# Performance work log

Hardware: AMD Instinct MI355X
Metric: run time of the kernel (lower is better)

The kernel has to match this reference:

```python
import jax, jax.numpy as jnp
import numpy as np

B, T, IN, H, NC = 2048, 128, 64, 256, 1


def setup_inputs() -> dict:
    key = jax.random.key(0)
    ks = jax.random.split(key, 7)
    s_ih = 1.0 / np.sqrt(H)
    return {
        "x": jax.random.normal(ks[0], (B, T, IN), dtype=jnp.float32),
        "W_ih": jax.random.normal(ks[1], (4 * H, IN), dtype=jnp.float32) * s_ih,
        "W_hh": jax.random.normal(ks[2], (4 * H, H), dtype=jnp.float32) * s_ih,
        "b_ih": jax.random.normal(ks[3], (4 * H,), dtype=jnp.float32) * s_ih,
        "b_hh": jax.random.normal(ks[4], (4 * H,), dtype=jnp.float32) * s_ih,
        "fc_W": jax.random.normal(ks[5], (NC, H), dtype=jnp.float32) * s_ih,
        "fc_b": jax.random.normal(ks[6], (NC,), dtype=jnp.float32) * s_ih,
    }


def _lstm_last_hidden(x, W_ih, W_hh, b_ih, b_hh):
    # Precompute input contribution for all timesteps: [B, T, 4H]
    xg = jnp.einsum('bti,gi->btg', x, W_ih) + (b_ih + b_hh)
    h0 = jnp.zeros((x.shape[0], H), dtype=x.dtype)
    c0 = jnp.zeros((x.shape[0], H), dtype=x.dtype)

    def step(carry, xg_t):
        h, c = carry
        gates = xg_t + h @ W_hh.T  # [B, 4H], PyTorch gate order i,f,g,o
        i, f, g, o = jnp.split(gates, 4, axis=-1)
        i = jax.nn.sigmoid(i)
        f = jax.nn.sigmoid(f)
        g = jnp.tanh(g)
        o = jax.nn.sigmoid(o)
        c = f * c + i * g
        h = o * jnp.tanh(c)
        return (h, c), None

    (h_last, _), _ = jax.lax.scan(step, (h0, c0), jnp.swapaxes(xg, 0, 1))
    return h_last  # [B, H]


def reference(x, W_ih, W_hh, b_ih, b_hh, fc_W, fc_b):
    h_last = _lstm_last_hidden(x, W_ih, W_hh, b_ih, b_hh)
    return h_last @ fc_W.T + fc_b  # [B, num_classes]
```

## Files before the change

kernel.cpp:

```cpp
#include <hip/hip_runtime.h>

typedef _Float16 half8 __attribute__((ext_vector_type(8)));
typedef float f32x4 __attribute__((ext_vector_type(4)));
typedef unsigned int u32x2 __attribute__((ext_vector_type(2)));

#define B_SZ   2048
#define T_SZ   128
#define IN_SZ  64
#define H_SZ   256
#define G4     1024
#define NB     8
#define NGRP   32
#define NTHR   512
#define KT_N   10
#define HPAD   36

__device__ __forceinline__ float sigmoidf_(float x) { return 1.0f / (1.0f + __expf(-x)); }
__device__ __forceinline__ float tanhf_(float x) { return 1.0f - 2.0f / (__expf(2.0f * x) + 1.0f); }

__global__ void prep_kernel(const float* __restrict__ W_ih, const float* __restrict__ W_hh,
                            const float* __restrict__ b_ih, const float* __restrict__ b_hh,
                            _Float16* __restrict__ Wr, float* __restrict__ biasr) {
  const int tid = blockIdx.x * blockDim.x + threadIdx.x;
  if (tid < G4) {
    const int TI = tid >> 4, m = tid & 15;
    const int q = m & 3, cs = m >> 2, nbk = TI >> 3, sub = TI & 7;
    const int grow = q * 256 + nbk * 32 + sub * 4 + cs;
    biasr[tid] = b_ih[grow] + b_hh[grow];
  }
  if (tid >= 64 * KT_N * 64) return;
  const int l = tid & 63, kt = (tid >> 6) % KT_N, TI = tid / (64 * KT_N);
  const int lm = l & 15, lk = l >> 4;
  const int q = lm & 3, cs = lm >> 2, nbk = TI >> 3, sub = TI & 7;
  const int grow = q * 256 + nbk * 32 + sub * 4 + cs;
  const int k0 = kt * 32 + lk * 8;
  _Float16 v[8];
  #pragma unroll
  for (int kk = 0; kk < 8; ++kk) {
    const int k = k0 + kk;
    v[kk] = (_Float16)((k < IN_SZ) ? W_ih[grow * IN_SZ + k] : W_hh[grow * H_SZ + k - IN_SZ]);
  }
  *(half8*)&Wr[((size_t)(TI * KT_N + kt) * 64 + l) * 8] = *(half8*)v;
}

__global__ __launch_bounds__(NTHR, 1)
void lstm_kernel(const float* __restrict__ x,
                 const _Float16* __restrict__ Wr,
                 const float* __restrict__ biasr,
                 const float* __restrict__ fcW,
                 _Float16* __restrict__ hbuf,
                 int* __restrict__ flags,
                 float* __restrict__ partial) {
  __shared__ __align__(16) _Float16 Wlds[8 * KT_N * 512];
  __shared__ __align__(16) _Float16 hslab[64][HPAD];

  const int tid = threadIdx.x;
  const int l = tid & 63;
  const int w = tid >> 6;
  const int lm = l & 15, lk = l >> 4;
  const int bt = w & 3, gh = w >> 2;
  const int g = blockIdx.x >> 3, nbk = blockIdx.x & 7;
  const int brow = g * 64 + bt * 16 + lm;

  #pragma unroll
  for (int rep = 0; rep < 10; ++rep) {
    const int u = rep * NTHR + tid;
    const int sub = u / 640, r2 = u % 640, kt = r2 >> 6, l2 = r2 & 63;
    *(half8*)&Wlds[((size_t)(sub * KT_N + kt) * 64 + l2) * 8] =
        *(const half8*)&Wr[(((size_t)(nbk * 8 + sub) * KT_N + kt) * 64 + l2) * 8];
  }

  f32x4 bias[4];
  #pragma unroll
  for (int ti = 0; ti < 4; ++ti)
    bias[ti] = *(const f32x4*)&biasr[(nbk * 8 + gh * 4 + ti) * 16 + lk * 4];

  const float* xlane = x + (size_t)brow * T_SZ * IN_SZ + lk * 8;
  const int hcolb = gh * 16 + lk;
  int* flagg = flags + g * T_SZ;

  __syncthreads();

  float cst[4] = {0.f, 0.f, 0.f, 0.f};

  #define WL(ti_, kt_) (*(const half8*)&Wlds[((size_t)((gh * 4 + (ti_)) * KT_N + (kt_)) * 64 + l) * 8])

  for (int t = 0; t < T_SZ; ++t) {
    const int par = t & 1;

    half8 bx0, bx1;
    {
      const float* xp = xlane + t * IN_SZ;
      const f32x4 a0 = *(const f32x4*)(xp);
      const f32x4 a1 = *(const f32x4*)(xp + 4);
      const f32x4 b0 = *(const f32x4*)(xp + 32);
      const f32x4 b1 = *(const f32x4*)(xp + 36);
      #pragma unroll
      for (int i = 0; i < 4; ++i) {
        bx0[i] = (_Float16)a0[i]; bx0[4 + i] = (_Float16)a1[i];
        bx1[i] = (_Float16)b0[i]; bx1[4 + i] = (_Float16)b1[i];
      }
    }

    f32x4 acc[4];
    #pragma unroll
    for (int ti = 0; ti < 4; ++ti) acc[ti] = bias[ti];

    #pragma unroll
    for (int ti = 0; ti < 4; ++ti)
      acc[ti] = __builtin_amdgcn_mfma_f32_16x16x32_f16(WL(ti, 0), bx0, acc[ti], 0, 0, 0);
    #pragma unroll
    for (int ti = 0; ti < 4; ++ti)
      acc[ti] = __builtin_amdgcn_mfma_f32_16x16x32_f16(WL(ti, 1), bx1, acc[ti], 0, 0, 0);

    if (t > 0) {
      if (tid == 0) {
        while (__hip_atomic_load(flagg + (t - 1), __ATOMIC_RELAXED, __HIP_MEMORY_SCOPE_AGENT) < NB)
          __builtin_amdgcn_s_sleep(2);
      }
      __syncthreads();

      const char* hb = (const char*)hbuf + (size_t)(par ^ 1) * (B_SZ * H_SZ * 2)
                       + (size_t)brow * (H_SZ * 2) + lk * 16;
      f32x4 hr0, hr1, hr2, hr3, hr4, hr5, hr6, hr7;
      asm volatile("global_load_dwordx4 %0, %1, off sc0 sc1"            : "=v"(hr0) : "v"(hb));
      asm volatile("global_load_dwordx4 %0, %1, off offset:64 sc0 sc1"  : "=v"(hr1) : "v"(hb));
      asm volatile("global_load_dwordx4 %0, %1, off offset:128 sc0 sc1" : "=v"(hr2) : "v"(hb));
      asm volatile("global_load_dwordx4 %0, %1, off offset:192 sc0 sc1" : "=v"(hr3) : "v"(hb));
      asm volatile("global_load_dwordx4 %0, %1, off offset:256 sc0 sc1" : "=v"(hr4) : "v"(hb));
      asm volatile("global_load_dwordx4 %0, %1, off offset:320 sc0 sc1" : "=v"(hr5) : "v"(hb));
      asm volatile("global_load_dwordx4 %0, %1, off offset:384 sc0 sc1" : "=v"(hr6) : "v"(hb));
      asm volatile("global_load_dwordx4 %0, %1, off offset:448 sc0 sc1" : "=v"(hr7) : "v"(hb));
      asm volatile("s_waitcnt vmcnt(0)"
                   : "+v"(hr0), "+v"(hr1), "+v"(hr2), "+v"(hr3),
                     "+v"(hr4), "+v"(hr5), "+v"(hr6), "+v"(hr7));
      __builtin_amdgcn_sched_barrier(0);

      #define HMK(kk_, hr_) { const half8 hh = __builtin_bit_cast(half8, hr_); \
        _Pragma("unroll") \
        for (int ti = 0; ti < 4; ++ti) \
          acc[ti] = __builtin_amdgcn_mfma_f32_16x16x32_f16(WL(ti, 2 + kk_), hh, acc[ti], 0, 0, 0); }
      HMK(0, hr0) HMK(1, hr1) HMK(2, hr2) HMK(3, hr3)
      HMK(4, hr4) HMK(5, hr5) HMK(6, hr6) HMK(7, hr7)
      #undef HMK
    }

    #pragma unroll
    for (int ti = 0; ti < 4; ++ti) {
      const float iv = sigmoidf_(acc[ti][0]);
      const float fv = sigmoidf_(acc[ti][1]);
      const float gv = tanhf_   (acc[ti][2]);
      const float ov = sigmoidf_(acc[ti][3]);
      const float cn = fv * cst[ti] + iv * gv;
      cst[ti] = cn;
      hslab[bt * 16 + lm][hcolb + ti * 4] = (_Float16)(ov * tanhf_(cn));
    }
    __syncthreads();

    if (t < T_SZ - 1) {
      {
        const int row = tid >> 3, c0 = (tid & 7) * 4;
        const u32x2 val = *(const u32x2*)&hslab[row][c0];
        char* dst = (char*)hbuf + (size_t)par * (B_SZ * H_SZ * 2)
                    + ((size_t)(g * 64 + row) * H_SZ + nbk * 32 + c0) * 2;
        asm volatile("global_store_dwordx2 %0, %1, off sc0 sc1" :: "v"(dst), "v"(val) : "memory");
      }
      asm volatile("s_waitcnt vmcnt(0)" ::: "memory");
      __syncthreads();
      if (tid == 0)
        __hip_atomic_fetch_add(flagg + t, 1, __ATOMIC_RELAXED, __HIP_MEMORY_SCOPE_AGENT);
    } else {
      if (tid < 64) {
        float p = 0.f;
        #pragma unroll
        for (int c = 0; c < 32; ++c)
          p += (float)hslab[tid][c] * fcW[nbk * 32 + c];
        partial[(size_t)nbk * B_SZ + g * 64 + tid] = p;
      }
    }
  }
  #undef WL
}

__global__ void fc_kernel(const float* __restrict__ partial, const float* __restrict__ fcb,
                          float* __restrict__ out) {
  const int b = blockIdx.x * 256 + threadIdx.x;
  if (b >= B_SZ) return;
  float s = fcb[0];
  #pragma unroll
  for (int n = 0; n < NB; ++n) s += partial[(size_t)n * B_SZ + b];
  out[b] = s;
}

extern "C" void kernel_launch(void* const* d_in, const int* in_sizes, int n_in,
                              void* d_out, int out_size, void* d_ws, size_t ws_size,
                              hipStream_t stream) {
  const float* x    = (const float*)d_in[0];
  const float* W_ih = (const float*)d_in[1];
  const float* W_hh = (const float*)d_in[2];
  const float* b_ih = (const float*)d_in[3];
  const float* b_hh = (const float*)d_in[4];
  const float* fcW  = (const float*)d_in[5];
  const float* fcb  = (const float*)d_in[6];
  float* out = (float*)d_out;

  char* ws = (char*)d_ws;
  _Float16* Wr   = (_Float16*)ws;
  float* biasr   = (float*)(ws + 655360);
  _Float16* hbuf = (_Float16*)(ws + 659456);
  int* flags     = (int*)(ws + 659456 + 2097152);
  float* partial = (float*)(ws + 659456 + 2097152 + 16384);

  hipMemsetAsync(flags, 0, NGRP * T_SZ * sizeof(int), stream);
  hipLaunchKernelGGL(prep_kernel, dim3(160), dim3(256), 0, stream,
                     W_ih, W_hh, b_ih, b_hh, Wr, biasr);
  hipLaunchKernelGGL(lstm_kernel, dim3(256), dim3(NTHR), 0, stream,
                     x, Wr, biasr, fcW, hbuf, flags, partial);
  hipLaunchKernelGGL(fc_kernel, dim3(8), dim3(256), 0, stream,
                     partial, fcb, out);
}
```

Baseline: 672.3 us.

## Permute gate rows so lanes store h directly, prefetch next x, drop LDS staging

The gate-row permutation in the prep kernel now gives each lane four contiguous hidden columns, so every lane writes its fp16 h slice straight to global memory and the LDS staging slab with its extra barrier goes away. The next timestep's x is loaded early and converted after the recurrent MFMAs, which hides global load latency behind the wait for the other blocks. Full __syncthreads is replaced by raw s_barrier, the spin sleep is shortened, and the final FC dot product is done from registers with shuffles plus a small LDS reduction. The risks are more scattered 8-byte global stores and relying on s_barrier without implicit memory fences.

```diff
diff --git a/kernel.cpp b/kernel.cpp
--- a/kernel.cpp
+++ b/kernel.cpp
@@ -1,6 +1,7 @@
 #include <hip/hip_runtime.h>
 
 typedef _Float16 half8 __attribute__((ext_vector_type(8)));
+typedef _Float16 half4 __attribute__((ext_vector_type(4)));
 typedef float f32x4 __attribute__((ext_vector_type(4)));
 typedef unsigned int u32x2 __attribute__((ext_vector_type(2)));
 
@@ -13,7 +14,6 @@
 #define NGRP   32
 #define NTHR   512
 #define KT_N   10
-#define HPAD   36
 
 __device__ __forceinline__ float sigmoidf_(float x) { return 1.0f / (1.0f + __expf(-x)); }
 __device__ __forceinline__ float tanhf_(float x) { return 1.0f - 2.0f / (__expf(2.0f * x) + 1.0f); }
@@ -25,14 +25,14 @@
   if (tid < G4) {
     const int TI = tid >> 4, m = tid & 15;
     const int q = m & 3, cs = m >> 2, nbk = TI >> 3, sub = TI & 7;
-    const int grow = q * 256 + nbk * 32 + sub * 4 + cs;
+    const int grow = q * 256 + nbk * 32 + (sub >> 2) * 16 + cs * 4 + (sub & 3);
     biasr[tid] = b_ih[grow] + b_hh[grow];
   }
   if (tid >= 64 * KT_N * 64) return;
   const int l = tid & 63, kt = (tid >> 6) % KT_N, TI = tid / (64 * KT_N);
   const int lm = l & 15, lk = l >> 4;
   const int q = lm & 3, cs = lm >> 2, nbk = TI >> 3, sub = TI & 7;
-  const int grow = q * 256 + nbk * 32 + sub * 4 + cs;
+  const int grow = q * 256 + nbk * 32 + (sub >> 2) * 16 + cs * 4 + (sub & 3);
   const int k0 = kt * 32 + lk * 8;
   _Float16 v[8];
   #pragma unroll
@@ -51,8 +51,8 @@
                  _Float16* __restrict__ hbuf,
                  int* __restrict__ flags,
                  float* __restrict__ partial) {
-  __shared__ __align__(16) _Float16 Wlds[8 * KT_N * 512];
-  __shared__ __align__(16) _Float16 hslab[64][HPAD];
+  __shared__ __align__(16) char smem[81920];
+  _Float16* Wlds = (_Float16*)smem;
 
   const int tid = threadIdx.x;
   const int l = tid & 63;
@@ -76,31 +76,33 @@
     bias[ti] = *(const f32x4*)&biasr[(nbk * 8 + gh * 4 + ti) * 16 + lk * 4];
 
   const float* xlane = x + (size_t)brow * T_SZ * IN_SZ + lk * 8;
-  const int hcolb = gh * 16 + lk;
+  const int colb = gh * 16 + lk * 4;
   int* flagg = flags + g * T_SZ;
 
   __syncthreads();
 
   float cst[4] = {0.f, 0.f, 0.f, 0.f};
+  float hvf[4] = {0.f, 0.f, 0.f, 0.f};
 
   #define WL(ti_, kt_) (*(const half8*)&Wlds[((size_t)((gh * 4 + (ti_)) * KT_N + (kt_)) * 64 + l) * 8])
+
+  half8 bx0, bx1;
+  {
+    const float* xp = xlane;
+    const f32x4 a0 = *(const f32x4*)(xp);
+    const f32x4 a1 = *(const f32x4*)(xp + 4);
+    const f32x4 b0 = *(const f32x4*)(xp + 32);
+    const f32x4 b1 = *(const f32x4*)(xp + 36);
+    #pragma unroll
+    for (int i = 0; i < 4; ++i) {
+      bx0[i] = (_Float16)a0[i]; bx0[4 + i] = (_Float16)a1[i];
+      bx1[i] = (_Float16)b0[i]; bx1[4 + i] = (_Float16)b1[i];
+    }
+  }
 
   for (int t = 0; t < T_SZ; ++t) {
     const int par = t & 1;
-
-    half8 bx0, bx1;
-    {
-      const float* xp = xlane + t * IN_SZ;
-      const f32x4 a0 = *(const f32x4*)(xp);
-      const f32x4 a1 = *(const f32x4*)(xp + 4);
-      const f32x4 b0 = *(const f32x4*)(xp + 32);
-      const f32x4 b1 = *(const f32x4*)(xp + 36);
-      #pragma unroll
-      for (int i = 0; i < 4; ++i) {
-        bx0[i] = (_Float16)a0[i]; bx0[4 + i] = (_Float16)a1[i];
-        bx1[i] = (_Float16)b0[i]; bx1[4 + i] = (_Float16)b1[i];
-      }
-    }
+    const bool hx = (t + 1 < T_SZ);
 
     f32x4 acc[4];
     #pragma unroll
@@ -112,13 +114,23 @@
     #pragma unroll
     for (int ti = 0; ti < 4; ++ti)
       acc[ti] = __builtin_amdgcn_mfma_f32_16x16x32_f16(WL(ti, 1), bx1, acc[ti], 0, 0, 0);
+
+    f32x4 xa0, xa1, xb0, xb1;
+    if (hx) {
+      const float* xp = xlane + (t + 1) * IN_SZ;
+      xa0 = *(const f32x4*)(xp);
+      xa1 = *(const f32x4*)(xp + 4);
+      xb0 = *(const f32x4*)(xp + 32);
+      xb1 = *(const f32x4*)(xp + 36);
+      asm volatile("" : "+v"(xa0), "+v"(xa1), "+v"(xb0), "+v"(xb1));
+    }
 
     if (t > 0) {
       if (tid == 0) {
         while (__hip_atomic_load(flagg + (t - 1), __ATOMIC_RELAXED, __HIP_MEMORY_SCOPE_AGENT) < NB)
-          __builtin_amdgcn_s_sleep(2);
+          __builtin_amdgcn_s_sleep(1);
       }
-      __syncthreads();
+      __builtin_amdgcn_s_barrier();
 
       const char* hb = (const char*)hbuf + (size_t)(par ^ 1) * (B_SZ * H_SZ * 2)
                        + (size_t)brow * (H_SZ * 2) + lk * 16;
@@ -145,6 +157,15 @@
       #undef HMK
     }
 
+    if (hx) {
+      #pragma unroll
+      for (int i = 0; i < 4; ++i) {
+        bx0[i] = (_Float16)xa0[i]; bx0[4 + i] = (_Float16)xa1[i];
+        bx1[i] = (_Float16)xb0[i]; bx1[4 + i] = (_Float16)xb1[i];
+      }
+    }
+
+    half4 hv4;
     #pragma unroll
     for (int ti = 0; ti < 4; ++ti) {
       const float iv = sigmoidf_(acc[ti][0]);
@@ -153,33 +174,36 @@
       const float ov = sigmoidf_(acc[ti][3]);
       const float cn = fv * cst[ti] + iv * gv;
       cst[ti] = cn;
-      hslab[bt * 16 + lm][hcolb + ti * 4] = (_Float16)(ov * tanhf_(cn));
-    }
-    __syncthreads();
-
-    if (t < T_SZ - 1) {
-      {
-        const int row = tid >> 3, c0 = (tid & 7) * 4;
-        const u32x2 val = *(const u32x2*)&hslab[row][c0];
-        char* dst = (char*)hbuf + (size_t)par * (B_SZ * H_SZ * 2)
-                    + ((size_t)(g * 64 + row) * H_SZ + nbk * 32 + c0) * 2;
-        asm volatile("global_store_dwordx2 %0, %1, off sc0 sc1" :: "v"(dst), "v"(val) : "memory");
-      }
+      const float hv = ov * tanhf_(cn);
+      hvf[ti] = hv;
+      hv4[ti] = (_Float16)hv;
+    }
+
+    if (hx) {
+      char* dst = (char*)hbuf + (size_t)par * (B_SZ * H_SZ * 2)
+                  + ((size_t)brow * H_SZ + nbk * 32 + colb) * 2;
+      const u32x2 val = __builtin_bit_cast(u32x2, hv4);
+      asm volatile("global_store_dwordx2 %0, %1, off sc0 sc1" :: "v"(dst), "v"(val) : "memory");
       asm volatile("s_waitcnt vmcnt(0)" ::: "memory");
-      __syncthreads();
+      __builtin_amdgcn_s_barrier();
       if (tid == 0)
         __hip_atomic_fetch_add(flagg + t, 1, __ATOMIC_RELAXED, __HIP_MEMORY_SCOPE_AGENT);
-    } else {
-      if (tid < 64) {
-        float p = 0.f;
-        #pragma unroll
-        for (int c = 0; c < 32; ++c)
-          p += (float)hslab[tid][c] * fcW[nbk * 32 + c];
-        partial[(size_t)nbk * B_SZ + g * 64 + tid] = p;
-      }
     }
   }
   #undef WL
+
+  __syncthreads();
+  float* fcred = (float*)smem;
+  float p = 0.f;
+  #pragma unroll
+  for (int ti = 0; ti < 4; ++ti)
+    p += hvf[ti] * fcW[nbk * 32 + colb + ti];
+  p += __shfl_xor(p, 16);
+  p += __shfl_xor(p, 32);
+  if (lk == 0) fcred[(bt * 16 + lm) * 2 + gh] = p;
+  __syncthreads();
+  if (tid < 64)
+    partial[(size_t)nbk * B_SZ + g * 64 + tid] = fcred[tid * 2 + 0] + fcred[tid * 2 + 1];
 }
 
 __global__ void fc_kernel(const float* __restrict__ partial, const float* __restrict__ fcb,
```

Measured after the change: 667.2 us. No clear change (-0.8%).
